# Optimization experiments

Hardware: AMD Instinct MI355X
Metric: run time of the kernel (lower is better)

## Reference

```python
import jax, jax.numpy as jnp
import numpy as np

N = 8192
K = 64

def setup_inputs() -> dict:
    key = jax.random.key(0)
    kw, ky = jax.random.split(key)
    W = jax.random.uniform(kw, (N, N), dtype=jnp.float32)
    Y = jax.random.normal(ky, (N, K), dtype=jnp.float32)
    return {"W": W, "Y": Y}

def reference(W, Y):
    # SpectralNetLoss(normalized=False):
    #   Dy[i,j] = ||y_i - y_j||^2 ; loss = sum(W * Dy) / (2n)
    n = Y.shape[0]
    sq = jnp.sum(Y * Y, axis=1)                      # (n,)
    # squared pairwise distances: ||y_i||^2 + ||y_j||^2 - 2 y_i.y_j
    Dy = sq[:, None] + sq[None, :] - 2.0 * (Y @ Y.T)  # (n, n)
    Dy = jnp.maximum(Dy, 0.0)  # clamp tiny negatives from cancellation (cdist is nonneg)
    loss = jnp.sum(W * Dy) / (2.0 * n)
    return loss
```

## Files before the change

kernel.cpp:

```cpp
#include <hip/hip_runtime.h>
#include <stdint.h>

#define N 8192
#define K 64
#define TILE 128

typedef __attribute__((ext_vector_type(8))) short bf16x8;
typedef __attribute__((ext_vector_type(4))) float floatx4;
typedef __attribute__((ext_vector_type(4))) unsigned short ushort4v;

__global__ __launch_bounds__(256) void prep_kernel(const float* __restrict__ Y,
                                                   unsigned short* __restrict__ Ybf,
                                                   float* __restrict__ sq,
                                                   float* __restrict__ out) {
    if (blockIdx.x == 0 && threadIdx.x == 0) out[0] = 0.0f;
    const int t = blockIdx.x * 256 + threadIdx.x;
    floatx4 v = *reinterpret_cast<const floatx4*>(Y + (size_t)t * 4);
    ushort4v o;
    #pragma unroll
    for (int e = 0; e < 4; ++e) {
        uint32_t bits = __float_as_uint(v[e]);
        uint32_t rnd  = bits + 0x7FFF + ((bits >> 16) & 1);
        o[e] = (unsigned short)(rnd >> 16);
    }
    *reinterpret_cast<ushort4v*>(Ybf + (size_t)t * 4) = o;
    float s = v[0]*v[0] + v[1]*v[1] + v[2]*v[2] + v[3]*v[3];
    #pragma unroll
    for (int m = 8; m >= 1; m >>= 1) s += __shfl_xor(s, m, 64);
    if ((threadIdx.x & 15) == 0) sq[t >> 4] = s;
}

__global__ __launch_bounds__(256) void loss_kernel(const float* __restrict__ W,
                                                   const unsigned short* __restrict__ Ybf,
                                                   const float* __restrict__ sq,
                                                   float* __restrict__ out) {
    __shared__ float wsum[4];

    const int i0   = (blockIdx.x >> 6) * TILE;
    const int j0   = (blockIdx.x & 63) * TILE;
    const int tid  = threadIdx.x;
    const int wv   = tid >> 6;
    const int lane = tid & 63;
    const int qRow = (wv >> 1) * 64;
    const int qCol = (wv & 1) * 64;
    const int laneM = lane & 15;
    const int kq    = lane >> 4;

    bf16x8 afrag[2][4], bfrag[2][4];
    #pragma unroll
    for (int ks = 0; ks < 2; ++ks) {
        #pragma unroll
        for (int mt = 0; mt < 4; ++mt) {
            const int rowA = i0 + qRow + mt * 16 + laneM;
            afrag[ks][mt] = *reinterpret_cast<const bf16x8*>(Ybf + (size_t)rowA * K + ks * 32 + kq * 8);
            const int rowB = j0 + qCol + mt * 16 + laneM;
            bfrag[ks][mt] = *reinterpret_cast<const bf16x8*>(Ybf + (size_t)rowB * K + ks * 32 + kq * 8);
        }
    }

    float   sqi[4];
    floatx4 sqj[4];
    #pragma unroll
    for (int mt = 0; mt < 4; ++mt)
        sqi[mt] = sq[i0 + qRow + mt * 16 + laneM];
    #pragma unroll
    for (int nt = 0; nt < 4; ++nt)
        sqj[nt] = *reinterpret_cast<const floatx4*>(sq + j0 + qCol + nt * 16 + kq * 4);

    floatx4 wf[4][4];
    #pragma unroll
    for (int mt = 0; mt < 4; ++mt) {
        const float* wrow = W + (size_t)(i0 + qRow + mt * 16 + laneM) * N + (j0 + qCol + kq * 4);
        #pragma unroll
        for (int nt = 0; nt < 4; ++nt)
            wf[mt][nt] = *reinterpret_cast<const floatx4*>(wrow + nt * 16);
    }

    floatx4 acc[4][4];
    #pragma unroll
    for (int mt = 0; mt < 4; ++mt)
        #pragma unroll
        for (int nt = 0; nt < 4; ++nt) acc[mt][nt] = (floatx4){0.f, 0.f, 0.f, 0.f};

    #pragma unroll
    for (int ks = 0; ks < 2; ++ks)
        #pragma unroll
        for (int mt = 0; mt < 4; ++mt)
            #pragma unroll
            for (int nt = 0; nt < 4; ++nt)
                acc[mt][nt] = __builtin_amdgcn_mfma_f32_16x16x32_bf16(bfrag[ks][nt], afrag[ks][mt], acc[mt][nt], 0, 0, 0);

    float p0 = 0.f, p1 = 0.f, p2 = 0.f, p3 = 0.f;
    #pragma unroll
    for (int mt = 0; mt < 4; ++mt) {
        const float si = sqi[mt];
        #pragma unroll
        for (int nt = 0; nt < 4; ++nt) {
            const floatx4 g = acc[mt][nt];
            const floatx4 w4 = wf[mt][nt];
            const floatx4 sj = sqj[nt];
            float d0 = fmaxf(si + sj[0] - 2.0f * g[0], 0.f);
            float d1 = fmaxf(si + sj[1] - 2.0f * g[1], 0.f);
            float d2 = fmaxf(si + sj[2] - 2.0f * g[2], 0.f);
            float d3 = fmaxf(si + sj[3] - 2.0f * g[3], 0.f);
            p0 = fmaf(w4[0], d0, p0);
            p1 = fmaf(w4[1], d1, p1);
            p2 = fmaf(w4[2], d2, p2);
            p3 = fmaf(w4[3], d3, p3);
        }
    }
    float partial = (p0 + p1) + (p2 + p3);

    #pragma unroll
    for (int m = 32; m >= 1; m >>= 1) partial += __shfl_xor(partial, m, 64);
    if (lane == 0) wsum[wv] = partial;
    __syncthreads();
    if (tid == 0) {
        float tot = (wsum[0] + wsum[1]) + (wsum[2] + wsum[3]);
        atomicAdd(out, tot * (1.0f / (2.0f * (float)N)));
    }
}

extern "C" void kernel_launch(void* const* d_in, const int* in_sizes, int n_in,
                              void* d_out, int out_size, void* d_ws, size_t ws_size,
                              hipStream_t stream) {
    const float* W = (const float*)d_in[0];
    const float* Y = (const float*)d_in[1];
    float* out = (float*)d_out;

    unsigned short* Ybf = (unsigned short*)d_ws;
    float* sq = (float*)((char*)d_ws + (size_t)N * K * 2);

    prep_kernel<<<(N * K / 4) / 256, 256, 0, stream>>>(Y, Ybf, sq, out);
    loss_kernel<<<(N / TILE) * (N / TILE), 256, 0, stream>>>(W, Ybf, sq, out);
}
```

Baseline: 361.0 us.

## Loop each block over eight column tiles with double-buffered W and Y prefetch

Each block now sweeps eight consecutive 128-wide column tiles for one row tile instead of handling a single tile. W chunks and the next tile's bf16 Y fragments are prefetched in a rotating register buffer while MFMAs and the weighted distance reduction run on the current tile. This cuts the grid from 4096 to 512 blocks, reuses the row fragments, and reduces atomic traffic. The risk is lower occupancy and fewer waves available to hide memory latency while streaming W.

```diff
diff --git a/kernel.cpp b/kernel.cpp
--- a/kernel.cpp
+++ b/kernel.cpp
@@ -4,6 +4,8 @@
 #define N 8192
 #define K 64
 #define TILE 128
+#define JT 8
+#define NSTEP (4 * JT)
 
 typedef __attribute__((ext_vector_type(8))) short bf16x8;
 typedef __attribute__((ext_vector_type(4))) float floatx4;
@@ -30,14 +32,14 @@
     if ((threadIdx.x & 15) == 0) sq[t >> 4] = s;
 }
 
-__global__ __launch_bounds__(256) void loss_kernel(const float* __restrict__ W,
-                                                   const unsigned short* __restrict__ Ybf,
-                                                   const float* __restrict__ sq,
-                                                   float* __restrict__ out) {
+__global__ __launch_bounds__(256, 2) void loss_kernel(const float* __restrict__ W,
+                                                      const unsigned short* __restrict__ Ybf,
+                                                      const float* __restrict__ sq,
+                                                      float* __restrict__ out) {
     __shared__ float wsum[4];
 
-    const int i0   = (blockIdx.x >> 6) * TILE;
-    const int j0   = (blockIdx.x & 63) * TILE;
+    const int i0   = (blockIdx.x >> 3) * TILE;
+    const int j0   = (blockIdx.x & 7) * (TILE * JT);
     const int tid  = threadIdx.x;
     const int wv   = tid >> 6;
     const int lane = tid & 63;
@@ -46,71 +48,83 @@
     const int laneM = lane & 15;
     const int kq    = lane >> 4;
 
-    bf16x8 afrag[2][4], bfrag[2][4];
+    bf16x8 afrag[2][4];
+    float  sqi[4];
     #pragma unroll
-    for (int ks = 0; ks < 2; ++ks) {
+    for (int mt = 0; mt < 4; ++mt) {
+        const int row = i0 + qRow + mt * 16 + laneM;
+        afrag[0][mt] = *reinterpret_cast<const bf16x8*>(Ybf + (size_t)row * K + kq * 8);
+        afrag[1][mt] = *reinterpret_cast<const bf16x8*>(Ybf + (size_t)row * K + 32 + kq * 8);
+        sqi[mt] = sq[row];
+    }
+
+    bf16x8  bfr[2][2][4];
+    floatx4 sqjb[2][4];
+    #pragma unroll
+    for (int nt = 0; nt < 4; ++nt) {
+        const int row = j0 + qCol + nt * 16 + laneM;
+        bfr[0][0][nt] = *reinterpret_cast<const bf16x8*>(Ybf + (size_t)row * K + kq * 8);
+        bfr[0][1][nt] = *reinterpret_cast<const bf16x8*>(Ybf + (size_t)row * K + 32 + kq * 8);
+        sqjb[0][nt]   = *reinterpret_cast<const floatx4*>(sq + j0 + qCol + nt * 16 + kq * 4);
+    }
+
+    const float* wl = W + (size_t)(i0 + qRow + laneM) * N + (j0 + qCol + kq * 4);
+
+    floatx4 wfb[4][4];
+    #pragma unroll
+    for (int g = 0; g < 4; ++g)
         #pragma unroll
-        for (int mt = 0; mt < 4; ++mt) {
-            const int rowA = i0 + qRow + mt * 16 + laneM;
-            afrag[ks][mt] = *reinterpret_cast<const bf16x8*>(Ybf + (size_t)rowA * K + ks * 32 + kq * 8);
-            const int rowB = j0 + qCol + mt * 16 + laneM;
-            bfrag[ks][mt] = *reinterpret_cast<const bf16x8*>(Ybf + (size_t)rowB * K + ks * 32 + kq * 8);
+        for (int nt = 0; nt < 4; ++nt)
+            wfb[g][nt] = *reinterpret_cast<const floatx4*>(wl + (size_t)g * 16 * N + nt * 16);
+
+    float p0 = 0.f, p1 = 0.f, p2 = 0.f, p3 = 0.f;
+
+    #pragma unroll
+    for (int s = 0; s < NSTEP; ++s) {
+        const int mt  = s & 3;
+        const int jt  = s >> 2;
+        const int buf = jt & 1;
+
+        if (mt == 0 && jt + 1 < JT) {
+            #pragma unroll
+            for (int nt = 0; nt < 4; ++nt) {
+                const int row = j0 + (jt + 1) * TILE + qCol + nt * 16 + laneM;
+                bfr[buf ^ 1][0][nt] = *reinterpret_cast<const bf16x8*>(Ybf + (size_t)row * K + kq * 8);
+                bfr[buf ^ 1][1][nt] = *reinterpret_cast<const bf16x8*>(Ybf + (size_t)row * K + 32 + kq * 8);
+                sqjb[buf ^ 1][nt]   = *reinterpret_cast<const floatx4*>(sq + j0 + (jt + 1) * TILE + qCol + nt * 16 + kq * 4);
+            }
+        }
+
+        floatx4 accv[4];
+        #pragma unroll
+        for (int nt = 0; nt < 4; ++nt) accv[nt] = (floatx4){0.f, 0.f, 0.f, 0.f};
+        #pragma unroll
+        for (int ks = 0; ks < 2; ++ks)
+            #pragma unroll
+            for (int nt = 0; nt < 4; ++nt)
+                accv[nt] = __builtin_amdgcn_mfma_f32_16x16x32_bf16(bfr[buf][ks][nt], afrag[ks][mt], accv[nt], 0, 0, 0);
+
+        const float si = sqi[mt];
+        #pragma unroll
+        for (int nt = 0; nt < 4; ++nt) {
+            const floatx4 g  = accv[nt];
+            const floatx4 w4 = wfb[s & 3][nt];
+            const floatx4 sj = sqjb[buf][nt];
+            p0 = fmaf(w4[0], fmaxf(si + sj[0] - 2.0f * g[0], 0.f), p0);
+            p1 = fmaf(w4[1], fmaxf(si + sj[1] - 2.0f * g[1], 0.f), p1);
+            p2 = fmaf(w4[2], fmaxf(si + sj[2] - 2.0f * g[2], 0.f), p2);
+            p3 = fmaf(w4[3], fmaxf(si + sj[3] - 2.0f * g[3], 0.f), p3);
+        }
+
+        if (s + 4 < NSTEP) {
+            #pragma unroll
+            for (int nt = 0; nt < 4; ++nt)
+                wfb[s & 3][nt] = *reinterpret_cast<const floatx4*>(
+                    wl + (size_t)mt * 16 * N + (jt + 1) * TILE + nt * 16);
         }
     }
 
-    float   sqi[4];
-    floatx4 sqj[4];
-    #pragma unroll
-    for (int mt = 0; mt < 4; ++mt)
-        sqi[mt] = sq[i0 + qRow + mt * 16 + laneM];
-    #pragma unroll
-    for (int nt = 0; nt < 4; ++nt)
-        sqj[nt] = *reinterpret_cast<const floatx4*>(sq + j0 + qCol + nt * 16 + kq * 4);
-
-    floatx4 wf[4][4];
-    #pragma unroll
-    for (int mt = 0; mt < 4; ++mt) {
-        const float* wrow = W + (size_t)(i0 + qRow + mt * 16 + laneM) * N + (j0 + qCol + kq * 4);
-        #pragma unroll
-        for (int nt = 0; nt < 4; ++nt)
-            wf[mt][nt] = *reinterpret_cast<const floatx4*>(wrow + nt * 16);
-    }
-
-    floatx4 acc[4][4];
-    #pragma unroll
-    for (int mt = 0; mt < 4; ++mt)
-        #pragma unroll
-        for (int nt = 0; nt < 4; ++nt) acc[mt][nt] = (floatx4){0.f, 0.f, 0.f, 0.f};
-
-    #pragma unroll
-    for (int ks = 0; ks < 2; ++ks)
-        #pragma unroll
-        for (int mt = 0; mt < 4; ++mt)
-            #pragma unroll
-            for (int nt = 0; nt < 4; ++nt)
-                acc[mt][nt] = __builtin_amdgcn_mfma_f32_16x16x32_bf16(bfrag[ks][nt], afrag[ks][mt], acc[mt][nt], 0, 0, 0);
-
-    float p0 = 0.f, p1 = 0.f, p2 = 0.f, p3 = 0.f;
-    #pragma unroll
-    for (int mt = 0; mt < 4; ++mt) {
-        const float si = sqi[mt];
-        #pragma unroll
-        for (int nt = 0; nt < 4; ++nt) {
-            const floatx4 g = acc[mt][nt];
-            const floatx4 w4 = wf[mt][nt];
-            const floatx4 sj = sqj[nt];
-            float d0 = fmaxf(si + sj[0] - 2.0f * g[0], 0.f);
-            float d1 = fmaxf(si + sj[1] - 2.0f * g[1], 0.f);
-            float d2 = fmaxf(si + sj[2] - 2.0f * g[2], 0.f);
-            float d3 = fmaxf(si + sj[3] - 2.0f * g[3], 0.f);
-            p0 = fmaf(w4[0], d0, p0);
-            p1 = fmaf(w4[1], d1, p1);
-            p2 = fmaf(w4[2], d2, p2);
-            p3 = fmaf(w4[3], d3, p3);
-        }
-    }
     float partial = (p0 + p1) + (p2 + p3);
-
     #pragma unroll
     for (int m = 32; m >= 1; m >>= 1) partial += __shfl_xor(partial, m, 64);
     if (lane == 0) wsum[wv] = partial;
@@ -132,5 +146,5 @@
     float* sq = (float*)((char*)d_ws + (size_t)N * K * 2);
 
     prep_kernel<<<(N * K / 4) / 256, 256, 0, stream>>>(Y, Ybf, sq, out);
-    loss_kernel<<<(N / TILE) * (N / TILE), 256, 0, stream>>>(W, Ybf, sq, out);
+    loss_kernel<<<(N / TILE) * (N / (TILE * JT)), 256, 0, stream>>>(W, Ybf, sq, out);
 }
```

New measurement: 376.8 us. +4.4%, slower.
